# Kernel optimization log

Hardware: AMD Instinct MI355X
Metric: run time of the kernel (lower is better)

Reference implementation:

```python
import jax, jax.numpy as jnp
import numpy as np

N = 20000
E = 320000
IN_CH = 512
OUT_CH = 256


def setup_inputs() -> dict:
    key = jax.random.key(0)
    ks = jax.random.split(key, 24)
    p = lambda k, shape: jax.random.normal(k, shape, jnp.float32) * 0.05
    return {
        "x": jax.random.normal(ks[0], (N, IN_CH), jnp.float32),
        "edge_index": jax.random.randint(ks[1], (2, E), 0, N),
        "original_size": 16384,
        "W1": p(ks[2], (IN_CH, 4 * 256)), "as1": p(ks[3], (4, 256)), "ad1": p(ks[4], (4, 256)), "b1": p(ks[5], (1024,)),
        "lw1": p(ks[6], (IN_CH, 1024)), "lb1": p(ks[7], (1024,)),
        "W2": p(ks[8], (1024, 4 * 256)), "as2": p(ks[9], (4, 256)), "ad2": p(ks[10], (4, 256)), "b2": p(ks[11], (1024,)),
        "lw2": p(ks[12], (1024, 1024)), "lb2": p(ks[13], (1024,)),
        "W3": p(ks[14], (1024, 6 * 256)), "as3": p(ks[15], (6, 256)), "ad3": p(ks[16], (6, 256)), "b3": p(ks[17], (256,)),
        "lw3": p(ks[18], (1024, OUT_CH)), "lb3": p(ks[19], (OUT_CH,)),
    }


def gat_conv(x, src, dst, W, a_src, a_dst, bias, heads, ch, concat):
    """PyG-style GATConv: gather -> edge attention -> segment softmax -> scatter-add."""
    n = x.shape[0]
    h = (x @ W).reshape(n, heads, ch)                      # [N,H,C]
    alpha_s = (h * a_src[None]).sum(-1)                    # [N,H]
    alpha_d = (h * a_dst[None]).sum(-1)                    # [N,H]
    e = jax.nn.leaky_relu(alpha_s[src] + alpha_d[dst], 0.2)  # [E,H]
    m = jax.ops.segment_max(e, dst, num_segments=n)        # per-dst max (stable softmax)
    e = jnp.exp(e - m[dst])
    denom = jax.ops.segment_sum(e, dst, num_segments=n)
    alpha = e / (denom[dst] + 1e-16)                       # [E,H]
    msg = h[src] * alpha[:, :, None]                       # [E,H,C]
    out = jax.ops.segment_sum(msg, dst, num_segments=n)    # [N,H,C]
    out = out.reshape(n, heads * ch) if concat else out.mean(axis=1)
    return out + bias


def reference(x, edge_index, original_size, W1, as1, ad1, b1, lw1, lb1,
              W2, as2, ad2, b2, lw2, lb2, W3, as3, ad3, b3, lw3, lb3):
    n = x.shape[0]
    loops = jnp.arange(n)
    src = jnp.concatenate([edge_index[0], loops])  # PyG add_self_loops=True default
    dst = jnp.concatenate([edge_index[1], loops])
    h = jax.nn.elu(gat_conv(x, src, dst, W1, as1, ad1, b1, 4, 256, True) + x @ lw1 + lb1)
    h = jax.nn.elu(gat_conv(h, src, dst, W2, as2, ad2, b2, 4, 256, True) + h @ lw2 + lb2)
    h = gat_conv(h, src, dst, W3, as3, ad3, b3, 6, 256, False) + h @ lw3 + lb3
    return h[:original_size]
```

## Files before the change

kernel.cpp:

```cpp
#include <hip/hip_runtime.h>

#define N_NODES 20000
#define M_PAD   20096
#define E_EDGES 320000
#define CAP     96

typedef unsigned short u16;
typedef unsigned int   u32;
typedef __attribute__((ext_vector_type(8))) short bf16x8;
typedef __attribute__((ext_vector_type(4))) float f32x4;
typedef __attribute__((ext_vector_type(4))) u32   u32x4;

__device__ __forceinline__ float bf2f(u16 u){
  u32 x = ((u32)u) << 16; float f; __builtin_memcpy(&f, &x, 4); return f;
}
__device__ __forceinline__ u16 f2bf(float f){
  u32 u; __builtin_memcpy(&u, &f, 4);
  u += 0x7fffu + ((u >> 16) & 1u);
  return (u16)(u >> 16);
}
__device__ __forceinline__ float lrelu(float x){ return x > 0.f ? x : 0.2f * x; }

__device__ __forceinline__ void gl_lds16(const void* g, void* l){
  __builtin_amdgcn_global_load_lds((const __attribute__((address_space(1))) void*)g,
                                   (__attribute__((address_space(3))) void*)l, 16, 0, 0);
}

__device__ __forceinline__ void acc8(float* acc, float w, u32x4 p){
#pragma unroll
  for (int d = 0; d < 4; d++){
    u32 u = p[d];
    acc[2 * d]     += w * bf2f((u16)(u & 0xffff));
    acc[2 * d + 1] += w * bf2f((u16)(u >> 16));
  }
}

__global__ void scatter_k(const int* __restrict__ ei, int* __restrict__ cnt, int* __restrict__ esrc){
  int i = blockIdx.x * 256 + threadIdx.x;
  if (i < E_EDGES){
    int d = ei[E_EDGES + i];
    int p = atomicAdd(&cnt[d], 1);
    if (p < CAP) esrc[d * CAP + p] = ei[i];
  }
}

__global__ void tcast_all(const float* __restrict__ W1, const float* __restrict__ lw1, u16* __restrict__ Wt1,
                          const float* __restrict__ W2, const float* __restrict__ lw2, u16* __restrict__ Wt2,
                          const float* __restrict__ W3, const float* __restrict__ lw3, u16* __restrict__ Wt3)
{
  __shared__ float tile[32][33];
  int b = blockIdx.x;
  const float* src; u16* dst; int Nc, n0, ldd;
  if      (b <  512){            src = W1;  Nc = 1024; dst = Wt1; n0 = 0;    ldd = 512;  }
  else if (b < 1024){ b -=  512; src = lw1; Nc = 1024; dst = Wt1; n0 = 1024; ldd = 512;  }
  else if (b < 2048){ b -= 1024; src = W2;  Nc = 1024; dst = Wt2; n0 = 0;    ldd = 1024; }
  else if (b < 3072){ b -= 2048; src = lw2; Nc = 1024; dst = Wt2; n0 = 1024; ldd = 1024; }
  else if (b < 4608){ b -= 3072; src = W3;  Nc = 1536; dst = Wt3; n0 = 0;    ldd = 1024; }
  else              { b -= 4608; src = lw3; Nc = 256;  dst = Wt3; n0 = 1536; ldd = 1024; }
  int gx = Nc / 32;
  int kb = (b / gx) * 32, nb = (b % gx) * 32;
  int tx = threadIdx.x, ty = threadIdx.y;
#pragma unroll
  for (int r = 0; r < 32; r += 8)
    tile[ty + r][tx] = src[(size_t)(kb + ty + r) * Nc + nb + tx];
  __syncthreads();
#pragma unroll
  for (int r = 0; r < 32; r += 8){
    int n = nb + ty + r;
    dst[(size_t)(n0 + n) * ldd + kb + tx] = f2bf(tile[tx][ty + r]);
  }
}

__global__ void castx_k(const float* __restrict__ x, u16* __restrict__ o, int realRows){
  int r = blockIdx.x, c = threadIdx.x * 2;
  float2 v = (r < realRows) ? *(const float2*)(x + (size_t)r * 512 + c) : make_float2(0.f, 0.f);
  u32 pk = ((u32)f2bf(v.y) << 16) | (u32)f2bf(v.x);
  *(u32*)(o + (size_t)r * 512 + c) = pk;
}

__global__ void zpad_k(u16* __restrict__ p, int n){
  int i = blockIdx.x * 256 + threadIdx.x; if (i < n) p[i] = 0;
}

__global__ __launch_bounds__(256, 2)
void gemm_bf16(const u16* __restrict__ A, const u16* __restrict__ Bt, u16* __restrict__ C,
               int N, int K,
               const float* __restrict__ a_s, const float* __restrict__ a_d,
               float* __restrict__ aS, float* __restrict__ aD, int H)
{
  __shared__ __attribute__((aligned(16))) u16 lAB[2][12288];
  const int tid  = threadIdx.x;
  const int wave = tid >> 6, lane = tid & 63;
  const int bn = blockIdx.x, bm = blockIdx.y;
  const int wm = (wave >> 1) * 64, wn = (wave & 1) * 128;

  const int srow  = wave * 16 + (lane >> 2);
  const int skcol = (lane & 3) * 8;
  const u16* Ag0 = A  + (size_t)(bm * 128 + srow) * K + skcol;
  const u16* Ag1 = Ag0 + (size_t)64 * K;
  const u16* Bg  = Bt + (size_t)(bn * 256 + srow) * K + skcol;
  const int woff = wave * 512;

  f32x4 acc[4][8] = {};

  {
    u16* a0 = &lAB[0][woff];
    u16* a1 = &lAB[0][2048 + woff];
    u16* bw = &lAB[0][4096 + woff];
    gl_lds16(Ag0, a0);
    gl_lds16(Ag1, a1);
#pragma unroll
    for (int c = 0; c < 4; c++)
      gl_lds16(Bg + (size_t)(c * 64) * K, bw + c * 2048);
  }

  for (int k0 = 0; k0 < K; k0 += 32){
    const int p = (k0 >> 5) & 1;
    __syncthreads();
    if (k0 + 32 < K){
      u16* a0 = &lAB[p ^ 1][woff];
      u16* a1 = &lAB[p ^ 1][2048 + woff];
      u16* bw = &lAB[p ^ 1][4096 + woff];
      gl_lds16(Ag0 + k0 + 32, a0);
      gl_lds16(Ag1 + k0 + 32, a1);
#pragma unroll
      for (int c = 0; c < 4; c++)
        gl_lds16(Bg + (size_t)(c * 64) * K + k0 + 32, bw + c * 2048);
    }
    const u16* lA = &lAB[p][0];
    const u16* lB = &lAB[p][4096];
    const int koff = (lane >> 4) * 8;
    const int rsel = lane & 15;
    bf16x8 af[4], bfr[8];
#pragma unroll
    for (int i = 0; i < 4; i++) af[i]  = *(const bf16x8*)&lA[(wm + i * 16 + rsel) * 32 + koff];
#pragma unroll
    for (int j = 0; j < 8; j++) bfr[j] = *(const bf16x8*)&lB[(wn + j * 16 + rsel) * 32 + koff];
#pragma unroll
    for (int i = 0; i < 4; i++)
#pragma unroll
      for (int j = 0; j < 8; j++)
        acc[i][j] = __builtin_amdgcn_mfma_f32_16x16x32_bf16(af[i], bfr[j], acc[i][j], 0, 0, 0);
  }

  const int r0 = (lane >> 4) * 4, cl = lane & 15;
#pragma unroll
  for (int i = 0; i < 4; i++)
#pragma unroll
    for (int j = 0; j < 8; j++){
      int row = bm * 128 + wm + i * 16 + r0;
      int col = bn * 256 + wn + j * 16 + cl;
      u16* cp = C + (size_t)row * N + col;
#pragma unroll
      for (int r = 0; r < 4; r++) cp[(size_t)r * N] = f2bf(acc[i][j][r]);
    }

  if (bn < H){
    __syncthreads();
    float* fa = (float*)&lAB[0][0];
    fa[tid]       = a_s[bn * 256 + tid];
    fa[256 + tid] = a_d[bn * 256 + tid];
    __syncthreads();
    float* fb = (float*)&lAB[1][0];
    const int q = lane >> 4;
#pragma unroll
    for (int i = 0; i < 4; i++)
#pragma unroll
      for (int r = 0; r < 4; r++){
        float ps = 0.f, pd = 0.f;
#pragma unroll
        for (int j = 0; j < 8; j++){
          float v = acc[i][j][r];
          int c = wn + j * 16 + cl;
          ps += v * fa[c];
          pd += v * fa[256 + c];
        }
#pragma unroll
        for (int m = 1; m < 16; m <<= 1){
          ps += __shfl_xor(ps, m, 64);
          pd += __shfl_xor(pd, m, 64);
        }
        if (cl == 0){
          int row = wm + i * 16 + q * 4 + r;
          fb[(wave & 1) * 128 + row]       = ps;
          fb[256 + (wave & 1) * 128 + row] = pd;
        }
      }
    __syncthreads();
    if (tid < 128){
      int row = bm * 128 + tid;
      aS[(size_t)row * 8 + bn] = fb[tid] + fb[128 + tid];
      aD[(size_t)row * 8 + bn] = fb[256 + tid] + fb[384 + tid];
    }
  }
}

__global__ __launch_bounds__(256)
void agg4w_k(const u16* __restrict__ HG, int ldH,
             const int* __restrict__ cnt, const int* __restrict__ esrc,
             const float* __restrict__ aS, const float* __restrict__ aD,
             const float* __restrict__ bias, const float* __restrict__ lbias,
             u16* __restrict__ outb)
{
  __shared__ float s_w[4][256];
  const int tid = threadIdx.x, lane = tid & 63, wv = tid >> 6;
  const int dst = blockIdx.x * 4 + wv;
  const int e0 = dst * CAP;
  int deg = cnt[dst]; deg = deg < CAP ? deg : CAP;
  const int nE = deg + 1;
  const float4 adv = *(const float4*)(aD + (size_t)dst * 8);

  int myS = dst;
  float ea = -1e30f, eb = -1e30f, ec = -1e30f, ed = -1e30f;
  if (lane < nE){
    myS = (lane == deg) ? dst : esrc[e0 + lane];
    float4 as = *(const float4*)(aS + (size_t)myS * 8);
    ea = lrelu(as.x + adv.x); eb = lrelu(as.y + adv.y);
    ec = lrelu(as.z + adv.z); ed = lrelu(as.w + adv.w);
  }
  float m0 = ea, m1 = eb, m2 = ec, m3 = ed;
  for (int i = lane + 64; i < nE; i += 64){
    int s = (i == deg) ? dst : esrc[e0 + i];
    float4 as = *(const float4*)(aS + (size_t)s * 8);
    m0 = fmaxf(m0, lrelu(as.x + adv.x)); m1 = fmaxf(m1, lrelu(as.y + adv.y));
    m2 = fmaxf(m2, lrelu(as.z + adv.z)); m3 = fmaxf(m3, lrelu(as.w + adv.w));
  }
#pragma unroll
  for (int off = 1; off < 64; off <<= 1){
    m0 = fmaxf(m0, __shfl_xor(m0, off)); m1 = fmaxf(m1, __shfl_xor(m1, off));
    m2 = fmaxf(m2, __shfl_xor(m2, off)); m3 = fmaxf(m3, __shfl_xor(m3, off));
  }

  float w0 = __expf(ea - m0), w1 = __expf(eb - m1);
  float w2 = __expf(ec - m2), w3 = __expf(ed - m3);
  float l0 = w0, l1 = w1, l2 = w2, l3 = w3;
  for (int i = lane + 64; i < nE; i += 64){
    int s = (i == deg) ? dst : esrc[e0 + i];
    float4 as = *(const float4*)(aS + (size_t)s * 8);
    l0 += __expf(lrelu(as.x + adv.x) - m0); l1 += __expf(lrelu(as.y + adv.y) - m1);
    l2 += __expf(lrelu(as.z + adv.z) - m2); l3 += __expf(lrelu(as.w + adv.w) - m3);
  }
#pragma unroll
  for (int off = 1; off < 64; off <<= 1){
    l0 += __shfl_xor(l0, off); l1 += __shfl_xor(l1, off);
    l2 += __shfl_xor(l2, off); l3 += __shfl_xor(l3, off);
  }
  float d0 = 1.f / (l0 + 1e-16f), d1 = 1.f / (l1 + 1e-16f);
  float d2 = 1.f / (l2 + 1e-16f), d3 = 1.f / (l3 + 1e-16f);
  *(float4*)&s_w[wv][lane * 4] = make_float4(w0 * d0, w1 * d1, w2 * d2, w3 * d3);
  __syncthreads();

  const int h = lane >> 4;
  const int ch0 = lane * 16;
  const float mh   = (h < 2) ? (h == 0 ? m0 : m1) : (h == 2 ? m2 : m3);
  const float dh   = (h < 2) ? (h == 0 ? d0 : d1) : (h == 2 ? d2 : d3);
  const float advh = (h < 2) ? (h == 0 ? adv.x : adv.y) : (h == 2 ? adv.z : adv.w);
  float acc[16] = {};
  const u16* HGc = HG + ch0;
  const int nF = nE < 64 ? nE : 64;
  for (int i = 0; i < nF; i += 8){
    int ss[8]; float ww[8];
#pragma unroll
    for (int u = 0; u < 8; u++){
      int idx = i + u;
      ss[u] = __shfl(myS, idx);
      ww[u] = s_w[wv][idx * 4 + h];
    }
    u32x4 p0[8], p1[8];
#pragma unroll
    for (int u = 0; u < 8; u++){
      const u16* r = HGc + (size_t)ss[u] * ldH;
      p0[u] = *(const u32x4*)r; p1[u] = *(const u32x4*)(r + 8);
    }
#pragma unroll
    for (int u = 0; u < 8; u++){ acc8(acc, ww[u], p0[u]); acc8(acc + 8, ww[u], p1[u]); }
  }
  for (int j = 64; j < nE; j++){
    int s = (j == deg) ? dst : esrc[e0 + j];
    float e = lrelu(aS[(size_t)s * 8 + h] + advh);
    float w = __expf(e - mh) * dh;
    const u16* r = HGc + (size_t)s * ldH;
    acc8(acc, w, *(const u32x4*)r); acc8(acc + 8, w, *(const u32x4*)(r + 8));
  }

  const u16* lr = HG + (size_t)dst * ldH + 1024 + ch0;
  u32x4 q0 = *(const u32x4*)lr, q1 = *(const u32x4*)(lr + 8);
  float lin[16];
#pragma unroll
  for (int d = 0; d < 4; d++){
    lin[2*d]     = bf2f((u16)(q0[d] & 0xffff)); lin[2*d+1]   = bf2f((u16)(q0[d] >> 16));
    lin[8+2*d]   = bf2f((u16)(q1[d] & 0xffff)); lin[8+2*d+1] = bf2f((u16)(q1[d] >> 16));
  }
  u32 o[8];
#pragma unroll
  for (int d = 0; d < 8; d++){
    float va = acc[2*d]   + bias[ch0 + 2*d]   + lin[2*d]   + lbias[ch0 + 2*d];
    float vb = acc[2*d+1] + bias[ch0 + 2*d+1] + lin[2*d+1] + lbias[ch0 + 2*d+1];
    va = va > 0.f ? va : __expf(va) - 1.f;
    vb = vb > 0.f ? vb : __expf(vb) - 1.f;
    o[d] = ((u32)f2bf(vb) << 16) | (u32)f2bf(va);
  }
  u16* op = outb + (size_t)dst * 1024 + ch0;
  *(u32x4*)op = *(u32x4*)o;
  *(u32x4*)(op + 8) = *(u32x4*)(o + 4);
}

__global__ __launch_bounds__(256)
void agg6w_k(const u16* __restrict__ HG, int ldH,
             const int* __restrict__ cnt, const int* __restrict__ esrc,
             const float* __restrict__ aS, const float* __restrict__ aD,
             const float* __restrict__ bias, const float* __restrict__ lbias,
             float* __restrict__ outf)
{
  __shared__ float s_w[4][400];
  const int tid = threadIdx.x, lane = tid & 63, wv = tid >> 6;
  const int dst = blockIdx.x * 4 + wv;
  const int e0 = dst * CAP;
  int deg = cnt[dst]; deg = deg < CAP ? deg : CAP;
  const int nE = deg + 1;

  const float* advp = aD + (size_t)dst * 8;
  float4 av4 = *(const float4*)advp; float2 av2 = *(const float2*)(advp + 4);
  float adv[6] = { av4.x, av4.y, av4.z, av4.w, av2.x, av2.y };

  int myS = dst;
  float e[6];
#pragma unroll
  for (int h = 0; h < 6; h++) e[h] = -1e30f;
  if (lane < nE){
    myS = (lane == deg) ? dst : esrc[e0 + lane];
    float4 a0 = *(const float4*)(aS + (size_t)myS * 8);
    float2 a1 = *(const float2*)(aS + (size_t)myS * 8 + 4);
    e[0] = lrelu(a0.x + adv[0]); e[1] = lrelu(a0.y + adv[1]);
    e[2] = lrelu(a0.z + adv[2]); e[3] = lrelu(a0.w + adv[3]);
    e[4] = lrelu(a1.x + adv[4]); e[5] = lrelu(a1.y + adv[5]);
  }
  float m[6];
#pragma unroll
  for (int h = 0; h < 6; h++) m[h] = e[h];
  for (int i = lane + 64; i < nE; i += 64){
    int s = (i == deg) ? dst : esrc[e0 + i];
    float4 a0 = *(const float4*)(aS + (size_t)s * 8);
    float2 a1 = *(const float2*)(aS + (size_t)s * 8 + 4);
    float t[6] = { a0.x, a0.y, a0.z, a0.w, a1.x, a1.y };
#pragma unroll
    for (int h = 0; h < 6; h++) m[h] = fmaxf(m[h], lrelu(t[h] + adv[h]));
  }
#pragma unroll
  for (int h = 0; h < 6; h++)
#pragma unroll
    for (int off = 1; off < 64; off <<= 1) m[h] = fmaxf(m[h], __shfl_xor(m[h], off));

  float w[6], l[6];
#pragma unroll
  for (int h = 0; h < 6; h++){ w[h] = __expf(e[h] - m[h]); l[h] = w[h]; }
  for (int i = lane + 64; i < nE; i += 64){
    int s = (i == deg) ? dst : esrc[e0 + i];
    float4 a0 = *(const float4*)(aS + (size_t)s * 8);
    float2 a1 = *(const float2*)(aS + (size_t)s * 8 + 4);
    float t[6] = { a0.x, a0.y, a0.z, a0.w, a1.x, a1.y };
#pragma unroll
    for (int h = 0; h < 6; h++) l[h] += __expf(lrelu(t[h] + adv[h]) - m[h]);
  }
#pragma unroll
  for (int h = 0; h < 6; h++)
#pragma unroll
    for (int off = 1; off < 64; off <<= 1) l[h] += __shfl_xor(l[h], off);
  float dv[6];
#pragma unroll
  for (int h = 0; h < 6; h++) dv[h] = (1.f / 6.f) / (l[h] + 1e-16f);
  float* swp = &s_w[wv][lane * 6];
  ((float2*)swp)[0] = make_float2(w[0] * dv[0], w[1] * dv[1]);
  ((float2*)swp)[1] = make_float2(w[2] * dv[2], w[3] * dv[3]);
  ((float2*)swp)[2] = make_float2(w[4] * dv[4], w[5] * dv[5]);
  if (lane < 16) s_w[wv][384 + lane] = 0.f;
  __syncthreads();

  const int li = lane & 31, half = lane >> 5;
  const int ch0 = li * 8;
  float acc[8] = {};
  const u16* HGc = HG + ch0;
  const int nF = nE < 64 ? nE : 64;
  for (int i = half; i < nF; i += 4){
    int j = i + 2;
    int s0 = __shfl(myS, i), s1 = __shfl(myS, j & 63);
    const float* w0p = &s_w[wv][i * 6];
    const float* w1p = &s_w[wv][j * 6];
    const u16* r0 = HGc + (size_t)s0 * ldH;
    const u16* r1 = HGc + (size_t)s1 * ldH;
    u32x4 q0[6], q1[6];
#pragma unroll
    for (int hh = 0; hh < 6; hh++){
      q0[hh] = *(const u32x4*)(r0 + hh * 256);
      q1[hh] = *(const u32x4*)(r1 + hh * 256);
    }
#pragma unroll
    for (int hh = 0; hh < 6; hh++){
      acc8(acc, w0p[hh], q0[hh]);
      acc8(acc, w1p[hh], q1[hh]);
    }
  }
  for (int j = 64 + half; j < nE; j += 2){
    int s = (j == deg) ? dst : esrc[e0 + j];
    float4 a0 = *(const float4*)(aS + (size_t)s * 8);
    float2 a1 = *(const float2*)(aS + (size_t)s * 8 + 4);
    float t[6] = { a0.x, a0.y, a0.z, a0.w, a1.x, a1.y };
    const u16* r = HGc + (size_t)s * ldH;
#pragma unroll
    for (int h = 0; h < 6; h++){
      float wt = __expf(lrelu(t[h] + adv[h]) - m[h]) * dv[h];
      u32x4 p = *(const u32x4*)(r + h * 256);
      acc8(acc, wt, p);
    }
  }
#pragma unroll
  for (int c = 0; c < 8; c++) acc[c] += __shfl_xor(acc[c], 32);

  if (lane < 32){
    u32x4 q = *(const u32x4*)(HG + (size_t)dst * ldH + 1536 + ch0);
    float lin[8];
#pragma unroll
    for (int d = 0; d < 4; d++){
      lin[2*d]   = bf2f((u16)(q[d] & 0xffff));
      lin[2*d+1] = bf2f((u16)(q[d] >> 16));
    }
    float4 b0 = *(const float4*)(bias + ch0),  b1 = *(const float4*)(bias + ch0 + 4);
    float4 c0 = *(const float4*)(lbias + ch0), c1 = *(const float4*)(lbias + ch0 + 4);
    float4 o0, o1;
    o0.x = acc[0] + b0.x + lin[0] + c0.x; o0.y = acc[1] + b0.y + lin[1] + c0.y;
    o0.z = acc[2] + b0.z + lin[2] + c0.z; o0.w = acc[3] + b0.w + lin[3] + c0.w;
    o1.x = acc[4] + b1.x + lin[4] + c1.x; o1.y = acc[5] + b1.y + lin[5] + c1.y;
    o1.z = acc[6] + b1.z + lin[6] + c1.z; o1.w = acc[7] + b1.w + lin[7] + c1.w;
    float* op = outf + (size_t)dst * 256 + ch0;
    *(float4*)op = o0;
    *(float4*)(op + 4) = o1;
  }
}

extern "C" void kernel_launch(void* const* d_in, const int* in_sizes, int n_in,
                              void* d_out, int out_size, void* d_ws, size_t ws_size,
                              hipStream_t stream)
{
  const float* x   = (const float*)d_in[0];
  const int*   ei  = (const int*)  d_in[1];
  const float* W1  = (const float*)d_in[3];
  const float* as1 = (const float*)d_in[4];
  const float* ad1 = (const float*)d_in[5];
  const float* b1  = (const float*)d_in[6];
  const float* lw1 = (const float*)d_in[7];
  const float* lb1 = (const float*)d_in[8];
  const float* W2  = (const float*)d_in[9];
  const float* as2 = (const float*)d_in[10];
  const float* ad2 = (const float*)d_in[11];
  const float* b2  = (const float*)d_in[12];
  const float* lw2 = (const float*)d_in[13];
  const float* lb2 = (const float*)d_in[14];
  const float* W3  = (const float*)d_in[15];
  const float* as3 = (const float*)d_in[16];
  const float* ad3 = (const float*)d_in[17];
  const float* b3  = (const float*)d_in[18];
  const float* lw3 = (const float*)d_in[19];
  const float* lb3 = (const float*)d_in[20];

  char* wp = (char*)d_ws;
  auto nxt = [&](size_t b) -> void* {
    void* p = (void*)wp; wp += (b + 255) & ~(size_t)255; return p;
  };
  u16*  Wt1  = (u16*) nxt((size_t)2048 * 512  * 2);
  u16*  Wt2  = (u16*) nxt((size_t)2048 * 1024 * 2);
  u16*  Wt3  = (u16*) nxt((size_t)1792 * 1024 * 2);
  u16*  Xb   = (u16*) nxt((size_t)M_PAD * 1024 * 2);
  u16*  HG   = (u16*) nxt((size_t)M_PAD * 2048 * 2);
  float* aS  = (float*)nxt((size_t)M_PAD * 8 * 4);
  float* aD  = (float*)nxt((size_t)M_PAD * 8 * 4);
  int*  cnt  = (int*)  nxt((size_t)N_NODES * 4);
  int*  esrc = (int*)  nxt((size_t)N_NODES * CAP * 4);

  hipMemsetAsync(cnt, 0, (size_t)N_NODES * 4, stream);
  scatter_k<<<(E_EDGES + 255) / 256, 256, 0, stream>>>(ei, cnt, esrc);

  tcast_all<<<4864, dim3(32, 8), 0, stream>>>(W1, lw1, Wt1, W2, lw2, Wt2, W3, lw3, Wt3);

  castx_k<<<M_PAD, 256, 0, stream>>>(x, Xb, N_NODES);
  zpad_k <<<(96 * 1024 + 255) / 256, 256, 0, stream>>>(Xb + (size_t)N_NODES * 1024, 96 * 1024);

  const int MT = M_PAD / 128;

  gemm_bf16<<<dim3(2048 / 256, MT), 256, 0, stream>>>(Xb, Wt1, HG, 2048, 512,  as1, ad1, aS, aD, 4);
  agg4w_k  <<<N_NODES / 4, 256, 0, stream>>>(HG, 2048, cnt, esrc, aS, aD, b1, lb1, Xb);

  gemm_bf16<<<dim3(2048 / 256, MT), 256, 0, stream>>>(Xb, Wt2, HG, 2048, 1024, as2, ad2, aS, aD, 4);
  agg4w_k  <<<N_NODES / 4, 256, 0, stream>>>(HG, 2048, cnt, esrc, aS, aD, b2, lb2, Xb);

  gemm_bf16<<<dim3(1792 / 256, MT), 256, 0, stream>>>(Xb, Wt3, HG, 1792, 1024, as3, ad3, aS, aD, 6);
  int outRows = out_size / 256;
  agg6w_k  <<<outRows / 4, 256, 0, stream>>>(HG, 1792, cnt, esrc, aS, aD, b3, lb3, (float*)d_out);

  (void)in_sizes; (void)n_in; (void)ws_size;
}
```

Baseline: 807.4 us.

## Double-buffer neighbor-row gathers into LDS with async global_load_lds in GAT aggregation

Both GAT aggregation kernels now fetch neighbor feature rows for the first 64 edges with asynchronous global-to-LDS loads. Each wave gets its own double buffer in LDS (4 edges per stage in the 4-head kernel, 2 in the 6-head kernel), and manual vmcnt waits let the next batch load while the current one is accumulated. The aim is to hide gather latency and cut vector-register pressure from holding many in-flight rows. In exchange, per-block LDS grows to tens of KB, which can limit occupancy, and each row now takes an extra LDS round trip.

```diff
diff --git a/kernel.cpp b/kernel.cpp
--- a/kernel.cpp
+++ b/kernel.cpp
@@ -10,6 +10,8 @@
 typedef __attribute__((ext_vector_type(8))) short bf16x8;
 typedef __attribute__((ext_vector_type(4))) float f32x4;
 typedef __attribute__((ext_vector_type(4))) u32   u32x4;
+
+#define WAITVM(N) __builtin_amdgcn_s_waitcnt(0xF70 | ((N) & 0xF) | (((N) & 0x30) << 10))
 
 __device__ __forceinline__ float bf2f(u16 u){
   u32 x = ((u32)u) << 16; float f; __builtin_memcpy(&f, &x, 4); return f;
@@ -203,6 +205,7 @@
              u16* __restrict__ outb)
 {
   __shared__ float s_w[4][256];
+  __shared__ __attribute__((aligned(16))) u16 s_stage[4][2][4096];
   const int tid = threadIdx.x, lane = tid & 63, wv = tid >> 6;
   const int dst = blockIdx.x * 4 + wv;
   const int e0 = dst * CAP;
@@ -256,30 +259,43 @@
   const float dh   = (h < 2) ? (h == 0 ? d0 : d1) : (h == 2 ? d2 : d3);
   const float advh = (h < 2) ? (h == 0 ? adv.x : adv.y) : (h == 2 ? adv.z : adv.w);
   float acc[16] = {};
-  const u16* HGc = HG + ch0;
   const int nF = nE < 64 ? nE : 64;
-  for (int i = 0; i < nF; i += 8){
-    int ss[8]; float ww[8];
-#pragma unroll
-    for (int u = 0; u < 8; u++){
-      int idx = i + u;
-      ss[u] = __shfl(myS, idx);
-      ww[u] = s_w[wv][idx * 4 + h];
-    }
-    u32x4 p0[8], p1[8];
-#pragma unroll
-    for (int u = 0; u < 8; u++){
-      const u16* r = HGc + (size_t)ss[u] * ldH;
-      p0[u] = *(const u32x4*)r; p1[u] = *(const u32x4*)(r + 8);
-    }
-#pragma unroll
-    for (int u = 0; u < 8; u++){ acc8(acc, ww[u], p0[u]); acc8(acc + 8, ww[u], p1[u]); }
+  const int nB = (nF + 3) >> 2;
+  u16* stg = &s_stage[wv][0][0];
+
+  auto issue4 = [&](int b){
+    u16* lb = stg + (b & 1) * 4096;
+    int base4 = b * 4;
+#pragma unroll
+    for (int k = 0; k < 8; k++){
+      int c = k * 64 + lane;
+      int e = base4 + (c >> 7);
+      int s = __shfl(myS, e);
+      const u16* g = HG + (size_t)s * ldH + (c & 127) * 8;
+      gl_lds16(g, lb + k * 512);
+    }
+  };
+
+  issue4(0);
+  for (int b = 0; b < nB; b++){
+    if (b + 1 < nB){ issue4(b + 1); WAITVM(8); }
+    else           { WAITVM(0); }
+    const u16* buf = stg + (b & 1) * 4096;
+#pragma unroll
+    for (int e = 0; e < 4; e++){
+      int idx = b * 4 + e;
+      float w = s_w[wv][idx * 4 + h];
+      const u16* row = buf + e * 1024 + lane * 16;
+      u32x4 p0 = *(const u32x4*)row;
+      u32x4 p1 = *(const u32x4*)(row + 8);
+      acc8(acc, w, p0); acc8(acc + 8, w, p1);
+    }
   }
   for (int j = 64; j < nE; j++){
     int s = (j == deg) ? dst : esrc[e0 + j];
     float e = lrelu(aS[(size_t)s * 8 + h] + advh);
     float w = __expf(e - mh) * dh;
-    const u16* r = HGc + (size_t)s * ldH;
+    const u16* r = HG + ch0 + (size_t)s * ldH;
     acc8(acc, w, *(const u32x4*)r); acc8(acc + 8, w, *(const u32x4*)(r + 8));
   }
 
@@ -312,7 +328,8 @@
              const float* __restrict__ bias, const float* __restrict__ lbias,
              float* __restrict__ outf)
 {
-  __shared__ float s_w[4][400];
+  __shared__ float s_w[4][384];
+  __shared__ __attribute__((aligned(16))) u16 s_stg[4][2][3072];
   const int tid = threadIdx.x, lane = tid & 63, wv = tid >> 6;
   const int dst = blockIdx.x * 4 + wv;
   const int e0 = dst * CAP;
@@ -373,31 +390,41 @@
   ((float2*)swp)[0] = make_float2(w[0] * dv[0], w[1] * dv[1]);
   ((float2*)swp)[1] = make_float2(w[2] * dv[2], w[3] * dv[3]);
   ((float2*)swp)[2] = make_float2(w[4] * dv[4], w[5] * dv[5]);
-  if (lane < 16) s_w[wv][384 + lane] = 0.f;
   __syncthreads();
 
   const int li = lane & 31, half = lane >> 5;
   const int ch0 = li * 8;
   float acc[8] = {};
-  const u16* HGc = HG + ch0;
   const int nF = nE < 64 ? nE : 64;
-  for (int i = half; i < nF; i += 4){
-    int j = i + 2;
-    int s0 = __shfl(myS, i), s1 = __shfl(myS, j & 63);
-    const float* w0p = &s_w[wv][i * 6];
-    const float* w1p = &s_w[wv][j * 6];
-    const u16* r0 = HGc + (size_t)s0 * ldH;
-    const u16* r1 = HGc + (size_t)s1 * ldH;
-    u32x4 q0[6], q1[6];
+  const int nB = (nF + 1) >> 1;
+  u16* stg = &s_stg[wv][0][0];
+
+  auto issue2 = [&](int b){
+    u16* lb = stg + (b & 1) * 3072;
+    int base2 = b * 2;
+#pragma unroll
+    for (int k = 0; k < 6; k++){
+      int c = k * 64 + lane;
+      int e2 = (c >= 192) ? 1 : 0;
+      int off = c - e2 * 192;
+      int s = __shfl(myS, base2 + e2);
+      const u16* g = HG + (size_t)s * ldH + off * 8;
+      gl_lds16(g, lb + k * 512);
+    }
+  };
+
+  issue2(0);
+  for (int b = 0; b < nB; b++){
+    if (b + 1 < nB){ issue2(b + 1); WAITVM(6); }
+    else           { WAITVM(0); }
+    const u16* buf = stg + (b & 1) * 3072;
+    int idx = b * 2 + half;
+    const float* wp6 = &s_w[wv][idx * 6];
+    const u16* row = buf + half * 1536 + li * 8;
 #pragma unroll
     for (int hh = 0; hh < 6; hh++){
-      q0[hh] = *(const u32x4*)(r0 + hh * 256);
-      q1[hh] = *(const u32x4*)(r1 + hh * 256);
-    }
-#pragma unroll
-    for (int hh = 0; hh < 6; hh++){
-      acc8(acc, w0p[hh], q0[hh]);
-      acc8(acc, w1p[hh], q1[hh]);
+      u32x4 p = *(const u32x4*)(row + hh * 256);
+      acc8(acc, wp6[hh], p);
     }
   }
   for (int j = 64 + half; j < nE; j += 2){
@@ -405,7 +432,7 @@
     float4 a0 = *(const float4*)(aS + (size_t)s * 8);
     float2 a1 = *(const float2*)(aS + (size_t)s * 8 + 4);
     float t[6] = { a0.x, a0.y, a0.z, a0.w, a1.x, a1.y };
-    const u16* r = HGc + (size_t)s * ldH;
+    const u16* r = HG + ch0 + (size_t)s * ldH;
 #pragma unroll
     for (int h = 0; h < 6; h++){
       float wt = __expf(lrelu(t[h] + adv[h]) - m[h]) * dv[h];
```

New measurement: 799.9 us. About the same (-0.9%).
